# Performance work log

Measured on AMD Instinct MI355X. Metric: run time of the kernel, lower is better.

The kernel has to match this reference:

```python
import jax, jax.numpy as jnp
import numpy as np

NEG_SLOPE = 0.2


def gat_layer(x, src, dst, W, att_src, att_dst, bias, n_nodes):
    # PyG GATConv (heads=1): h = x @ W; per-edge logit = LeakyReLU(a_src.h[src] + a_dst.h[dst]);
    # softmax over edges grouped by destination node; out[d] = sum alpha * h[src] + bias.
    h = x @ W                                  # [N, F]
    a_s = h @ att_src                          # [N]
    a_d = h @ att_dst                          # [N]
    e = a_s[src] + a_d[dst]                    # [E]
    e = jnp.where(e > 0, e, NEG_SLOPE * e)     # leaky_relu
    m = jax.ops.segment_max(e, dst, num_segments=n_nodes)   # [N]
    w = jnp.exp(e - m[dst])                    # [E]
    z = jax.ops.segment_sum(w, dst, num_segments=n_nodes)   # [N]
    alpha = w / z[dst]                         # [E] (self-loops guarantee z>0)
    out = jax.ops.segment_sum(alpha[:, None] * h[src], dst, num_segments=n_nodes)
    return out + bias


def setup_inputs() -> dict:
    key = jax.random.key(0)
    ks = jax.random.split(key, 10)
    N, E, C_IN, H1, H2 = 100000, 3200000, 128, 50, 40
    x = jax.random.normal(ks[0], (N, C_IN), dtype=jnp.float32)
    edge_index = jax.random.randint(ks[1], (2, E), 0, N, dtype=jnp.int64)
    g1 = 1.0 / np.sqrt(C_IN)
    g2 = 1.0 / np.sqrt(H1)
    return {
        "x": x,
        "edge_index": edge_index,
        "W1": jax.random.normal(ks[2], (C_IN, H1), dtype=jnp.float32) * g1,
        "att_src1": jax.random.normal(ks[3], (H1,), dtype=jnp.float32) * g2,
        "att_dst1": jax.random.normal(ks[4], (H1,), dtype=jnp.float32) * g2,
        "bias1": jnp.zeros((H1,), dtype=jnp.float32),
        "W2": jax.random.normal(ks[5], (H1, H2), dtype=jnp.float32) * g2,
        "att_src2": jax.random.normal(ks[6], (H2,), dtype=jnp.float32) / np.sqrt(H2),
        "att_dst2": jax.random.normal(ks[7], (H2,), dtype=jnp.float32) / np.sqrt(H2),
        "bias2": jnp.zeros((H2,), dtype=jnp.float32),
    }


def reference(x, edge_index, W1, att_src1, att_dst1, bias1, W2, att_src2, att_dst2, bias2):
    n_nodes = x.shape[0]
    # PyG GATConv default add_self_loops=True: append (i, i) for every node.
    loop = jnp.arange(n_nodes, dtype=edge_index.dtype)
    src = jnp.concatenate([edge_index[0], loop])
    dst = jnp.concatenate([edge_index[1], loop])
    h = jax.nn.relu(gat_layer(x, src, dst, W1, att_src1, att_dst1, bias1, n_nodes))
    h = jax.nn.relu(gat_layer(h, src, dst, W2, att_src2, att_dst2, bias2, n_nodes))
    return h, edge_index
```

## Files before the change

kernel.cpp:

```cpp
#include <hip/hip_runtime.h>
#include <hip/hip_bf16.h>
#include <math.h>

#define NEG_SLOPE 0.2f
#define RBITS 8
#define RNODES 256
#define CHUNK 8192
#define CAP   9216
#define HS    32
#define HOS   52


__device__ __forceinline__ float waveReduceSum(float v) {
    #pragma unroll
    for (int off = 32; off > 0; off >>= 1) v += __shfl_xor(v, off);
    return v;
}

__device__ __forceinline__ unsigned pack_bf16(float a, float b) {
    __hip_bfloat162 p(__float2bfloat16(a), __float2bfloat16(b));
    return *reinterpret_cast<unsigned*>(&p);
}
__device__ __forceinline__ float bf16lo_f(unsigned u) { return __uint_as_float(u << 16); }
__device__ __forceinline__ float bf16hi_f(unsigned u) { return __uint_as_float(u & 0xFFFF0000u); }


__global__ void prep(const float* __restrict__ W1, float* __restrict__ WT1,
                     const float* __restrict__ W2, float* __restrict__ WT2,
                     int* __restrict__ bcursor,
                     int K1, int F1, int KP1, int FP1,
                     int K2, int F2, int KP2, int FP2, int NB) {
    int i = blockIdx.x * blockDim.x + threadIdx.x;
    int z1 = FP1 * KP1, z2 = FP2 * KP2;
    if (i < z1) {
        int f = i / KP1, k = i - f * KP1;
        WT1[i] = (f < F1 && k < K1) ? W1[k * F1 + f] : 0.f;
    } else if (i < z1 + z2) {
        int j = i - z1;
        int f = j / KP2, k = j - f * KP2;
        WT2[j] = (f < F2 && k < K2) ? W2[k * F2 + f] : 0.f;
    } else if (i < z1 + z2 + NB) {
        bcursor[i - z1 - z2] = 0;
    }
}


__global__ __launch_bounds__(512) void binning(
        const int* __restrict__ src, const int* __restrict__ dst,
        int* __restrict__ bcursor, int* __restrict__ binned,
        long E, int N, long TOT) {
    __shared__ int hist[512];
    __shared__ int base[512];
    int t = threadIdx.x;
    hist[t] = 0;
    __syncthreads();
    long c0 = blockIdx.x * (long)CHUNK;
    long c1 = c0 + CHUNK; if (c1 > TOT) c1 = TOT;
    for (long i = c0 + t; i < c1; i += 512) {
        int d = (i < E) ? dst[i] : (int)(i - E);
        atomicAdd(&hist[d >> RBITS], 1);
    }
    __syncthreads();
    {
        int c = hist[t];
        base[t] = c ? atomicAdd(&bcursor[t], c) : 0;
        hist[t] = 0;
    }
    __syncthreads();
    for (long i = c0 + t; i < c1; i += 512) {
        int s, d;
        if (i < E) { s = src[i]; d = dst[i]; } else { s = d = (int)(i - E); }
        int b = d >> RBITS;
        int p = base[b] + atomicAdd(&hist[b], 1);
        if (p >= CAP) p = CAP - 1;
        binned[(long)b * CAP + p] = ((d & (RNODES - 1)) << 17) | s;
    }
}

__global__ __launch_bounds__(512) void bucket_scan(
        const int* __restrict__ bcursor, int* __restrict__ bstarts,
        int* __restrict__ starts, int NB, int N, int TOT) {
    __shared__ int s[512];
    int t = threadIdx.x;
    int v = (t < NB) ? bcursor[t] : 0;
    s[t] = v;
    __syncthreads();
    for (int off = 1; off < 512; off <<= 1) {
        int u = (t >= off) ? s[t - off] : 0;
        __syncthreads();
        s[t] += u;
        __syncthreads();
    }
    int excl = s[t] - v;
    if (t < NB) bstarts[t] = excl;
    if (t == 0) { bstarts[NB] = TOT; starts[N] = TOT; }
}

__global__ __launch_bounds__(512) void bucket_csr(
        const int* __restrict__ binned, const int* __restrict__ bstarts,
        int* __restrict__ starts, int* __restrict__ csr_src, int N) {
    __shared__ int cnt[RNODES];
    __shared__ int scn[RNODES];
    int b = blockIdx.x, t = threadIdx.x;
    int node0 = b << RBITS;
    int R = N - node0; if (R > RNODES) R = RNODES;
    int e0 = bstarts[b];
    int ecnt = bstarts[b + 1] - e0;
    const int* bin = binned + (long)b * CAP;
    if (t < RNODES) cnt[t] = 0;
    __syncthreads();
    for (int i = t; i < ecnt; i += 512)
        atomicAdd(&cnt[bin[i] >> 17], 1);
    __syncthreads();
    int v = (t < RNODES) ? cnt[t] : 0;
    if (t < RNODES) scn[t] = v;
    __syncthreads();
    for (int off = 1; off < RNODES; off <<= 1) {
        int u = (t >= off && t < RNODES) ? scn[t - off] : 0;
        __syncthreads();
        if (t < RNODES) scn[t] += u;
        __syncthreads();
    }
    if (t < RNODES) {
        int excl = scn[t] - v;
        if (t < R) starts[node0 + t] = e0 + excl;
        cnt[t] = excl;
    }
    __syncthreads();
    for (int i = t; i < ecnt; i += 512) {
        int packed = bin[i];
        int ld = packed >> 17;
        int p = atomicAdd(&cnt[ld], 1);
        csr_src[e0 + p] = packed & 0x1FFFF;
    }
}

template <int KP, int F, int FPH, int XS>
__global__ __launch_bounds__(512) void gemm_tile(
        const float* __restrict__ x, const float* __restrict__ WT,
        const float* __restrict__ att_s, const float* __restrict__ att_d,
        unsigned* __restrict__ hb, float* __restrict__ as_, float* __restrict__ ad_,
        int N) {
    static_assert(KP % 4 == 0 && XS % 4 == 0 && XS >= KP, "vec4 staging");
    constexpr int Q4 = KP / 4;
    constexpr int RS = KP + 4;
    __shared__ float xT[64 * RS];
    __shared__ float asl[64], adl[64];
    int t = threadIdx.x;
    int lane = t & 63;
    int w = t >> 6;
    long n0 = (long)blockIdx.x * 64;
    int n = (int)n0 + lane;

    if (t < 64) { asl[t] = 0.f; adl[t] = 0.f; }
    for (int idx = t; idx < Q4 * 64; idx += 512) {
        int nn = idx / Q4;
        int k4 = (idx - nn * Q4) * 4;
        float4 v = make_float4(0.f, 0.f, 0.f, 0.f);
        if (n0 + nn < N) v = *(const float4*)(x + (n0 + nn) * (long)XS + k4);
        *(float4*)(xT + nn * RS + k4) = v;
    }
    __syncthreads();

    int f0 = __builtin_amdgcn_readfirstlane(w * 8);
    float acc[8] = {0.f, 0.f, 0.f, 0.f, 0.f, 0.f, 0.f, 0.f};
    if (f0 < F) {
        const float* xrow = xT + lane * RS;
        const float* wbase = WT + (long)f0 * KP;
        for (int k0 = 0; k0 < KP; k0 += 4) {
            float4 xv = *(const float4*)(xrow + k0);
            #pragma unroll
            for (int j = 0; j < 8; ++j) {
                const float* wr = wbase + j * KP + k0;
                float a = acc[j];
                a = fmaf(wr[0], xv.x, a);
                a = fmaf(wr[1], xv.y, a);
                a = fmaf(wr[2], xv.z, a);
                a = fmaf(wr[3], xv.w, a);
                acc[j] = a;
            }
        }
        float ps = 0.f, pd = 0.f;
        #pragma unroll
        for (int j = 0; j < 8; ++j) {
            float sa = (f0 + j < F) ? att_s[f0 + j] : 0.f;
            float da = (f0 + j < F) ? att_d[f0 + j] : 0.f;
            ps = fmaf(acc[j], sa, ps);
            pd = fmaf(acc[j], da, pd);
        }
        atomicAdd(&asl[lane], ps);
        atomicAdd(&adl[lane], pd);
    }
    __syncthreads();

    if (f0 < F && n < N) {
        int f0h = f0 >> 1;
        #pragma unroll
        for (int q = 0; q < 4; ++q) {
            int fp = f0h + q;
            if (fp < FPH) hb[(long)n * HS + fp] = pack_bf16(acc[2 * q], acc[2 * q + 1]);
        }
    }
    if (w == 0 && n < N) { as_[n] = asl[lane]; ad_[n] = adl[lane]; }
}

template <int F, int OST>
__global__ __launch_bounds__(64) void gat_gather(
                           const int* __restrict__ csr_src, const int* __restrict__ starts,
                           const float* __restrict__ as_, const float* __restrict__ ad_,
                           const unsigned* __restrict__ hb, const float* __restrict__ bias,
                           float* __restrict__ out, int N) {
    constexpr int NU4 = (F + 7) / 8;
    int lane = threadIdx.x & 63;
    int g  = lane >> 3;
    int fl = lane & 7;
    bool actf = (fl < NU4);
    long wave = (blockIdx.x * (long)blockDim.x + threadIdx.x) >> 6;
    if (wave >= N) return;
    int d = (int)wave;
    int s0 = starts[d], s1 = starts[d + 1];
    float add = ad_[d];
    const unsigned* hbase = hb + 4 * fl;

    float lsum = 0.f;
    float a0 = 0.f, a1 = 0.f, a2 = 0.f, a3 = 0.f;
    float a4 = 0.f, a5 = 0.f, a6 = 0.f, a7 = 0.f;

    for (int base = s0; base < s1; base += 64) {
        int k = base + lane;
        int s = (k < s1) ? csr_src[k] : 0;
        unsigned soff = (unsigned)s << 5;
        float e = as_[s] + add;
        e = e > 0.f ? e : NEG_SLOPE * e;
        float w = (k < s1) ? __expf(e) : 0.f;
        lsum += w;
        int cnt = min(64, s1 - base);
        int nst = (cnt + 7) >> 3;
        int j = 0;
        for (; j + 4 <= nst; j += 4) {
            int i0 = 8 * j + g;
            unsigned so0 = __shfl(soff, i0);
            unsigned so1 = __shfl(soff, i0 + 8);
            unsigned so2 = __shfl(soff, i0 + 16);
            unsigned so3 = __shfl(soff, i0 + 24);
            uint4 h0 = make_uint4(0u,0u,0u,0u), h1 = h0, h2 = h0, h3 = h0;
            if (actf) {
                h0 = *(const uint4*)(hbase + so0);
                h1 = *(const uint4*)(hbase + so1);
                h2 = *(const uint4*)(hbase + so2);
                h3 = *(const uint4*)(hbase + so3);
            }
            float w0 = __shfl(w, i0);
            float w1 = __shfl(w, i0 + 8);
            float w2 = __shfl(w, i0 + 16);
            float w3 = __shfl(w, i0 + 24);
            a0 = fmaf(w0, bf16lo_f(h0.x), a0); a1 = fmaf(w0, bf16hi_f(h0.x), a1);
            a2 = fmaf(w0, bf16lo_f(h0.y), a2); a3 = fmaf(w0, bf16hi_f(h0.y), a3);
            a4 = fmaf(w0, bf16lo_f(h0.z), a4); a5 = fmaf(w0, bf16hi_f(h0.z), a5);
            a6 = fmaf(w0, bf16lo_f(h0.w), a6); a7 = fmaf(w0, bf16hi_f(h0.w), a7);
            a0 = fmaf(w1, bf16lo_f(h1.x), a0); a1 = fmaf(w1, bf16hi_f(h1.x), a1);
            a2 = fmaf(w1, bf16lo_f(h1.y), a2); a3 = fmaf(w1, bf16hi_f(h1.y), a3);
            a4 = fmaf(w1, bf16lo_f(h1.z), a4); a5 = fmaf(w1, bf16hi_f(h1.z), a5);
            a6 = fmaf(w1, bf16lo_f(h1.w), a6); a7 = fmaf(w1, bf16hi_f(h1.w), a7);
            a0 = fmaf(w2, bf16lo_f(h2.x), a0); a1 = fmaf(w2, bf16hi_f(h2.x), a1);
            a2 = fmaf(w2, bf16lo_f(h2.y), a2); a3 = fmaf(w2, bf16hi_f(h2.y), a3);
            a4 = fmaf(w2, bf16lo_f(h2.z), a4); a5 = fmaf(w2, bf16hi_f(h2.z), a5);
            a6 = fmaf(w2, bf16lo_f(h2.w), a6); a7 = fmaf(w2, bf16hi_f(h2.w), a7);
            a0 = fmaf(w3, bf16lo_f(h3.x), a0); a1 = fmaf(w3, bf16hi_f(h3.x), a1);
            a2 = fmaf(w3, bf16lo_f(h3.y), a2); a3 = fmaf(w3, bf16hi_f(h3.y), a3);
            a4 = fmaf(w3, bf16lo_f(h3.z), a4); a5 = fmaf(w3, bf16hi_f(h3.z), a5);
            a6 = fmaf(w3, bf16lo_f(h3.w), a6); a7 = fmaf(w3, bf16hi_f(h3.w), a7);
        }
        for (; j < nst; ++j) {
            int idx = 8 * j + g;
            float wp = __shfl(w, idx);
            unsigned so = __shfl(soff, idx);
            if (actf) {
                uint4 hv = *(const uint4*)(hbase + so);
                a0 = fmaf(wp, bf16lo_f(hv.x), a0); a1 = fmaf(wp, bf16hi_f(hv.x), a1);
                a2 = fmaf(wp, bf16lo_f(hv.y), a2); a3 = fmaf(wp, bf16hi_f(hv.y), a3);
                a4 = fmaf(wp, bf16lo_f(hv.z), a4); a5 = fmaf(wp, bf16hi_f(hv.z), a5);
                a6 = fmaf(wp, bf16lo_f(hv.w), a6); a7 = fmaf(wp, bf16hi_f(hv.w), a7);
            }
        }
    }

    #pragma unroll
    for (int off = 8; off < 64; off <<= 1) {
        a0 += __shfl_xor(a0, off); a1 += __shfl_xor(a1, off);
        a2 += __shfl_xor(a2, off); a3 += __shfl_xor(a3, off);
        a4 += __shfl_xor(a4, off); a5 += __shfl_xor(a5, off);
        a6 += __shfl_xor(a6, off); a7 += __shfl_xor(a7, off);
    }
    float l = waveReduceSum(lsum);

    if (actf) {
        float inv = 1.f / l;
        int fb = 8 * fl;
        float v[8] = {a0, a1, a2, a3, a4, a5, a6, a7};
        float2* orow = (float2*)(out + (long)d * OST + fb);
        #pragma unroll
        for (int i = 0; i < 8; i += 2) {
            if (fb + i < OST) {
                float u0 = 0.f, u1 = 0.f;
                if (fb + i < F) {
                    u0 = v[i]     * inv + bias[fb + i];
                    u1 = v[i + 1] * inv + bias[fb + i + 1];
                    u0 = u0 > 0.f ? u0 : 0.f;
                    u1 = u1 > 0.f ? u1 : 0.f;
                }
                orow[i >> 1] = make_float2(u0, u1);
            }
        }
    }
}

__global__ void copy_edges4(const int4* __restrict__ ei, float4* __restrict__ out, long n4) {
    long i = blockIdx.x * (long)blockDim.x + threadIdx.x;
    if (i < n4) {
        int4 v = ei[i];
        out[i] = make_float4((float)v.x, (float)v.y, (float)v.z, (float)v.w);
    }
}
__global__ void copy_edges_tail(const int* __restrict__ ei, float* __restrict__ out,
                                long lo, long n) {
    long i = lo + blockIdx.x * (long)blockDim.x + threadIdx.x;
    if (i < n) out[i] = (float)ei[i];
}


extern "C" void kernel_launch(void* const* d_in, const int* in_sizes, int n_in,
                              void* d_out, int out_size, void* d_ws, size_t ws_size,
                              hipStream_t stream) {
    const float* x         = (const float*)d_in[0];
    const int*   edge_idx  = (const int*)d_in[1];
    const float* W1        = (const float*)d_in[2];
    const float* att_src1  = (const float*)d_in[3];
    const float* att_dst1  = (const float*)d_in[4];
    const float* bias1     = (const float*)d_in[5];
    const float* W2        = (const float*)d_in[6];
    const float* att_src2  = (const float*)d_in[7];
    const float* att_dst2  = (const float*)d_in[8];
    const float* bias2     = (const float*)d_in[9];

    const int  CIN = 128, F1 = 50, F2 = 40;
    const int  KP1 = 128, FP1 = 56;
    const int  KP2 = 52,  FP2 = 40;
    const int  N = in_sizes[0] / CIN;
    const long E = in_sizes[1] / 2;
    const int* src = edge_idx;
    const int* dst = edge_idx + E;
    const long TOT = E + N;
    const int  NB = (N + RNODES - 1) >> RBITS;

    char* wsb = (char*)d_ws;
    size_t regionA = (size_t)NB * CAP * 4;
    if ((size_t)N * HS * 4 > regionA) regionA = (size_t)N * HS * 4;
    int*      binned = (int*)wsb;
    unsigned* hb     = (unsigned*)wsb;
    float*    hout   = (float*)(wsb + regionA);
    float*    as_    = hout + (long)N * HOS;
    float*    ad_    = as_ + N;
    int*      starts  = (int*)(ad_ + N);
    int*      csr_src = starts + (N + 1);
    int*      bstarts = csr_src + TOT;
    int*      bcursor = bstarts + (NB + 1);
    float*    WT1     = (float*)(bcursor + NB + 3);
    float*    WT2     = WT1 + FP1 * KP1;

    float* out_h = (float*)d_out;
    float* out_e = out_h + (long)N * F2;

    const int B = 256;
    const int nTileBlocks = (N + 63) / 64;
    const int nBinBlocks = (int)((TOT + CHUNK - 1) / CHUNK);
    const int prepElems = FP1 * KP1 + FP2 * KP2 + NB;

    prep<<<dim3((prepElems + B - 1) / B), dim3(B), 0, stream>>>(
        W1, WT1, W2, WT2, bcursor, CIN, F1, KP1, FP1, F1, F2, KP2, FP2, NB);
    binning<<<dim3(nBinBlocks), dim3(512), 0, stream>>>(src, dst, bcursor, binned, E, N, TOT);
    bucket_scan<<<dim3(1), dim3(512), 0, stream>>>(bcursor, bstarts, starts, NB, N, (int)TOT);
    bucket_csr<<<dim3(NB), dim3(512), 0, stream>>>(binned, bstarts, starts, csr_src, N);

    gemm_tile<KP1, F1, FP1 / 2, CIN><<<dim3(nTileBlocks), dim3(512), 0, stream>>>(
        x, WT1, att_src1, att_dst1, hb, as_, ad_, N);
    gat_gather<F1, HOS><<<dim3(N), dim3(64), 0, stream>>>(
        csr_src, starts, as_, ad_, hb, bias1, hout, N);

    gemm_tile<KP2, F2, FP2 / 2, HOS><<<dim3(nTileBlocks), dim3(512), 0, stream>>>(
        hout, WT2, att_src2, att_dst2, hb, as_, ad_, N);
    gat_gather<F2, F2><<<dim3(N), dim3(64), 0, stream>>>(
        csr_src, starts, as_, ad_, hb, bias2, out_h, N);

    long n_e = 2 * E;
    long n4  = n_e / 4;
    copy_edges4<<<dim3((int)((n4 + B - 1) / B)), dim3(B), 0, stream>>>((const int4*)edge_idx, (float4*)out_e, n4);
    if (n_e - n4 * 4 > 0)
        copy_edges_tail<<<dim3(1), dim3(B), 0, stream>>>(edge_idx, out_e, n4 * 4, n_e);
}
```

Measured before the change: 371.3 us.

## Fuse edge-index output copy into binning and drop hidden-row padding

The separate kernels that convert edge_index to float output are removed, and binning writes the converted src and dst values while it already holds them in registers. This avoids re-reading the 25.6 MB edge array and saves a launch. The intermediate hidden buffer stride shrinks from 52 to 50 floats, so the layer-2 GEMM staging switches to float2 loads and the gather writes unpadded rows. The cost is that binning now does scattered extra stores per edge, and the narrower float2 staging may load less efficiently.

Measured after the change: 377.8 us. About the same (+1.8%).

```diff
diff --git a/kernel.cpp b/kernel.cpp
--- a/kernel.cpp
+++ b/kernel.cpp
@@ -8,7 +8,7 @@
 #define CHUNK 8192
 #define CAP   9216
 #define HS    32
-#define HOS   52
+#define HOS   50
 
 
 __device__ __forceinline__ float waveReduceSum(float v) {
@@ -48,7 +48,7 @@
 __global__ __launch_bounds__(512) void binning(
         const int* __restrict__ src, const int* __restrict__ dst,
         int* __restrict__ bcursor, int* __restrict__ binned,
-        long E, int N, long TOT) {
+        float* __restrict__ oe, long E, int N, long TOT) {
     __shared__ int hist[512];
     __shared__ int base[512];
     int t = threadIdx.x;
@@ -74,6 +74,7 @@
         int p = base[b] + atomicAdd(&hist[b], 1);
         if (p >= CAP) p = CAP - 1;
         binned[(long)b * CAP + p] = ((d & (RNODES - 1)) << 17) | s;
+        if (i < E) { oe[i] = (float)s; oe[E + i] = (float)d; }
     }
 }
 
@@ -141,8 +142,7 @@
         const float* __restrict__ att_s, const float* __restrict__ att_d,
         unsigned* __restrict__ hb, float* __restrict__ as_, float* __restrict__ ad_,
         int N) {
-    static_assert(KP % 4 == 0 && XS % 4 == 0 && XS >= KP, "vec4 staging");
-    constexpr int Q4 = KP / 4;
+    static_assert(KP % 4 == 0 && XS % 2 == 0 && KP >= XS, "staging");
     constexpr int RS = KP + 4;
     __shared__ float xT[64 * RS];
     __shared__ float asl[64], adl[64];
@@ -153,12 +153,24 @@
     int n = (int)n0 + lane;
 
     if (t < 64) { asl[t] = 0.f; adl[t] = 0.f; }
-    for (int idx = t; idx < Q4 * 64; idx += 512) {
-        int nn = idx / Q4;
-        int k4 = (idx - nn * Q4) * 4;
-        float4 v = make_float4(0.f, 0.f, 0.f, 0.f);
-        if (n0 + nn < N) v = *(const float4*)(x + (n0 + nn) * (long)XS + k4);
-        *(float4*)(xT + nn * RS + k4) = v;
+    if constexpr (XS % 4 == 0) {
+        constexpr int Q4 = KP / 4;
+        for (int idx = t; idx < Q4 * 64; idx += 512) {
+            int nn = idx / Q4;
+            int k4 = (idx - nn * Q4) * 4;
+            float4 v = make_float4(0.f, 0.f, 0.f, 0.f);
+            if (n0 + nn < N) v = *(const float4*)(x + (n0 + nn) * (long)XS + k4);
+            *(float4*)(xT + nn * RS + k4) = v;
+        }
+    } else {
+        constexpr int Q2 = KP / 2;
+        for (int idx = t; idx < Q2 * 64; idx += 512) {
+            int nn = idx / Q2;
+            int k2 = (idx - nn * Q2) * 2;
+            float2 v = make_float2(0.f, 0.f);
+            if (n0 + nn < N && k2 < XS) v = *(const float2*)(x + (n0 + nn) * (long)XS + k2);
+            *(float2*)(xT + nn * RS + k2) = v;
+        }
     }
     __syncthreads();
 
@@ -204,7 +216,7 @@
     if (w == 0 && n < N) { as_[n] = asl[lane]; ad_[n] = adl[lane]; }
 }
 
-template <int F, int OST>
+template <int F>
 __global__ __launch_bounds__(64) void gat_gather(
                            const int* __restrict__ csr_src, const int* __restrict__ starts,
                            const float* __restrict__ as_, const float* __restrict__ ad_,
@@ -298,34 +310,18 @@
         float inv = 1.f / l;
         int fb = 8 * fl;
         float v[8] = {a0, a1, a2, a3, a4, a5, a6, a7};
-        float2* orow = (float2*)(out + (long)d * OST + fb);
+        float2* orow = (float2*)(out + (long)d * F + fb);
         #pragma unroll
         for (int i = 0; i < 8; i += 2) {
-            if (fb + i < OST) {
-                float u0 = 0.f, u1 = 0.f;
-                if (fb + i < F) {
-                    u0 = v[i]     * inv + bias[fb + i];
-                    u1 = v[i + 1] * inv + bias[fb + i + 1];
-                    u0 = u0 > 0.f ? u0 : 0.f;
-                    u1 = u1 > 0.f ? u1 : 0.f;
-                }
+            if (fb + i < F) {
+                float u0 = v[i]     * inv + bias[fb + i];
+                float u1 = v[i + 1] * inv + bias[fb + i + 1];
+                u0 = u0 > 0.f ? u0 : 0.f;
+                u1 = u1 > 0.f ? u1 : 0.f;
                 orow[i >> 1] = make_float2(u0, u1);
             }
         }
     }
-}
-
-__global__ void copy_edges4(const int4* __restrict__ ei, float4* __restrict__ out, long n4) {
-    long i = blockIdx.x * (long)blockDim.x + threadIdx.x;
-    if (i < n4) {
-        int4 v = ei[i];
-        out[i] = make_float4((float)v.x, (float)v.y, (float)v.z, (float)v.w);
-    }
-}
-__global__ void copy_edges_tail(const int* __restrict__ ei, float* __restrict__ out,
-                                long lo, long n) {
-    long i = lo + blockIdx.x * (long)blockDim.x + threadIdx.x;
-    if (i < n) out[i] = (float)ei[i];
 }
 
 
@@ -378,23 +374,17 @@
 
     prep<<<dim3((prepElems + B - 1) / B), dim3(B), 0, stream>>>(
         W1, WT1, W2, WT2, bcursor, CIN, F1, KP1, FP1, F1, F2, KP2, FP2, NB);
-    binning<<<dim3(nBinBlocks), dim3(512), 0, stream>>>(src, dst, bcursor, binned, E, N, TOT);
+    binning<<<dim3(nBinBlocks), dim3(512), 0, stream>>>(src, dst, bcursor, binned, out_e, E, N, TOT);
     bucket_scan<<<dim3(1), dim3(512), 0, stream>>>(bcursor, bstarts, starts, NB, N, (int)TOT);
     bucket_csr<<<dim3(NB), dim3(512), 0, stream>>>(binned, bstarts, starts, csr_src, N);
 
     gemm_tile<KP1, F1, FP1 / 2, CIN><<<dim3(nTileBlocks), dim3(512), 0, stream>>>(
         x, WT1, att_src1, att_dst1, hb, as_, ad_, N);
-    gat_gather<F1, HOS><<<dim3(N), dim3(64), 0, stream>>>(
+    gat_gather<F1><<<dim3(N), dim3(64), 0, stream>>>(
         csr_src, starts, as_, ad_, hb, bias1, hout, N);
 
     gemm_tile<KP2, F2, FP2 / 2, HOS><<<dim3(nTileBlocks), dim3(512), 0, stream>>>(
         hout, WT2, att_src2, att_dst2, hb, as_, ad_, N);
-    gat_gather<F2, F2><<<dim3(N), dim3(64), 0, stream>>>(
+    gat_gather<F2><<<dim3(N), dim3(64), 0, stream>>>(
         csr_src, starts, as_, ad_, hb, bias2, out_h, N);
-
-    long n_e = 2 * E;
-    long n4  = n_e / 4;
-    copy_edges4<<<dim3((int)((n4 + B - 1) / B)), dim3(B), 0, stream>>>((const int4*)edge_idx, (float4*)out_e, n4);
-    if (n_e - n4 * 4 > 0)
-        copy_edges_tail<<<dim3(1), dim3(B), 0, stream>>>(edge_idx, out_e, n4 * 4, n_e);
-}
+}
```
